# Optimization experiments

Hardware: AMD Instinct MI355X
Metric: run time of the kernel (lower is better)

Reference implementation:

```python
import jax, jax.numpy as jnp
import numpy as np

N_CID = 10000
N_TIME = 10000
SEQ_LEN = 4096
STATE_LEN = 4096


def setup_inputs() -> dict:
    key = jax.random.key(0)
    k1, k2, k3 = jax.random.split(key, 3)
    history = jax.random.randint(k1, (SEQ_LEN,), 0, N_TIME, dtype=jnp.int64)
    current = jax.random.randint(k2, (STATE_LEN,), 0, N_CID, dtype=jnp.int64)
    cid_time = jax.random.normal(k3, (N_CID, N_TIME), dtype=jnp.float32)
    return {"history": history, "current": current, "cid_time": cid_time}


def reference(history, current, cid_time):
    # Vectorized form of the double loop:
    # attn_energies[i, j] = cid_time[current[i], history[j]]
    attn_energies = cid_time[current][:, history]  # [state_len, seq_len]
    # F.softmax with no dim on a 2-D tensor -> softmax over last dim
    return jax.nn.softmax(attn_energies, axis=-1)
```

## Files before the change

kernel.cpp:

```cpp
#include <hip/hip_runtime.h>


constexpr int SEQ_LEN   = 4096;
constexpr int STATE_LEN = 4096;
constexpr int N_TIME    = 10000;
constexpr int THREADS   = 256;
constexpr int VPT       = SEQ_LEN / THREADS;
constexpr int V4PT      = VPT / 4;
constexpr int ROW_F4    = N_TIME / 4;

__global__ __launch_bounds__(THREADS) void attn_cid_time_kernel(
    const int*   __restrict__ history,
    const int*   __restrict__ current,
    const float* __restrict__ cid_time,
    float*       __restrict__ out)
{
    __shared__ float row[N_TIME];
    __shared__ float red[4];

    const int t   = threadIdx.x;
    const int rid = blockIdx.x;

    int4 hidx[V4PT];
    const int4* __restrict__ h4 = reinterpret_cast<const int4*>(history);
#pragma unroll
    for (int k = 0; k < V4PT; ++k)
        hidx[k] = h4[t + k * THREADS];

    const long long cid = (long long)current[rid];
    const float4* __restrict__ s4 =
        reinterpret_cast<const float4*>(cid_time + cid * (long long)N_TIME);
    float4* __restrict__ row4 = reinterpret_cast<float4*>(row);
    for (int i = t; i < ROW_F4; i += THREADS)
        row4[i] = s4[i];
    __syncthreads();

    float v[VPT];
    float m = -3.402823466e+38f;
#pragma unroll
    for (int k = 0; k < V4PT; ++k) {
        v[4*k + 0] = row[hidx[k].x];
        v[4*k + 1] = row[hidx[k].y];
        v[4*k + 2] = row[hidx[k].z];
        v[4*k + 3] = row[hidx[k].w];
        m = fmaxf(m, fmaxf(fmaxf(v[4*k+0], v[4*k+1]), fmaxf(v[4*k+2], v[4*k+3])));
    }

#pragma unroll
    for (int off = 32; off >= 1; off >>= 1)
        m = fmaxf(m, __shfl_xor(m, off, 64));
    const int wid  = t >> 6;
    const int lane = t & 63;
    if (lane == 0) red[wid] = m;
    __syncthreads();
    m = fmaxf(fmaxf(red[0], red[1]), fmaxf(red[2], red[3]));
    __syncthreads();

    float s = 0.0f;
#pragma unroll
    for (int k = 0; k < VPT; ++k) {
        const float e = __expf(v[k] - m);
        v[k] = e;
        s += e;
    }

#pragma unroll
    for (int off = 32; off >= 1; off >>= 1)
        s += __shfl_xor(s, off, 64);
    if (lane == 0) red[wid] = s;
    __syncthreads();
    s = (red[0] + red[1]) + (red[2] + red[3]);
    const float inv = 1.0f / s;

    float4* __restrict__ dst4 =
        reinterpret_cast<float4*>(out + (long long)rid * SEQ_LEN);
#pragma unroll
    for (int k = 0; k < V4PT; ++k) {
        float4 o;
        o.x = v[4*k + 0] * inv;
        o.y = v[4*k + 1] * inv;
        o.z = v[4*k + 2] * inv;
        o.w = v[4*k + 3] * inv;
        dst4[t + k * THREADS] = o;
    }
}

extern "C" void kernel_launch(void* const* d_in, const int* in_sizes, int n_in,
                              void* d_out, int out_size, void* d_ws, size_t ws_size,
                              hipStream_t stream) {
    const int*   history  = (const int*)d_in[0];
    const int*   current  = (const int*)d_in[1];
    const float* cid_time = (const float*)d_in[2];
    float*       out      = (float*)d_out;

    attn_cid_time_kernel<<<STATE_LEN, THREADS, 0, stream>>>(history, current, cid_time, out);
}
```

Before: 488.0 us.

## Stage gathered rows via global_load_lds and double block size to 512 threads

Each cid_time row is now copied straight from global memory into LDS with the 16-byte global_load_lds builtin, one 1 KB chunk per wave, plus a scalar tail loop for the leftover elements. This removes the round trip through VGPRs and the separate LDS store. The block grows from 256 to 512 threads with a launch-bounds occupancy hint, so more waves are in flight per row, and the reductions now loop over all eight waves. The cost is that each thread holds fewer values, and correctness relies on the compiler waiting for the async LDS loads before the barrier.

```diff
diff --git a/kernel.cpp b/kernel.cpp
--- a/kernel.cpp
+++ b/kernel.cpp
@@ -1,25 +1,32 @@
 #include <hip/hip_runtime.h>
 
 
-constexpr int SEQ_LEN   = 4096;
-constexpr int STATE_LEN = 4096;
-constexpr int N_TIME    = 10000;
-constexpr int THREADS   = 256;
-constexpr int VPT       = SEQ_LEN / THREADS;
-constexpr int V4PT      = VPT / 4;
-constexpr int ROW_F4    = N_TIME / 4;
+constexpr int SEQ_LEN    = 4096;
+constexpr int STATE_LEN  = 4096;
+constexpr int N_TIME     = 10000;
+constexpr int THREADS    = 512;
+constexpr int NWAVES     = THREADS / 64;
+constexpr int VPT        = SEQ_LEN / THREADS;
+constexpr int V4PT       = VPT / 4;
+constexpr int ROW_BYTES  = N_TIME * 4;
+constexpr int CHUNK      = 64 * 16;
+constexpr int NFULL      = ROW_BYTES / CHUNK;
+constexpr int TAIL_BASE  = (NFULL * CHUNK) / 4;
+constexpr int TAIL_ELEMS = N_TIME - TAIL_BASE;
 
-__global__ __launch_bounds__(THREADS) void attn_cid_time_kernel(
+__global__ __launch_bounds__(THREADS, 8) void attn_cid_time_kernel(
     const int*   __restrict__ history,
     const int*   __restrict__ current,
     const float* __restrict__ cid_time,
     float*       __restrict__ out)
 {
-    __shared__ float row[N_TIME];
-    __shared__ float red[4];
+    __shared__ alignas(16) float row[N_TIME];
+    __shared__ float red[NWAVES];
 
-    const int t   = threadIdx.x;
-    const int rid = blockIdx.x;
+    const int t    = threadIdx.x;
+    const int rid  = blockIdx.x;
+    const int wid  = t >> 6;
+    const int lane = t & 63;
 
     int4 hidx[V4PT];
     const int4* __restrict__ h4 = reinterpret_cast<const int4*>(history);
@@ -28,11 +35,18 @@
         hidx[k] = h4[t + k * THREADS];
 
     const long long cid = (long long)current[rid];
-    const float4* __restrict__ s4 =
-        reinterpret_cast<const float4*>(cid_time + cid * (long long)N_TIME);
-    float4* __restrict__ row4 = reinterpret_cast<float4*>(row);
-    for (int i = t; i < ROW_F4; i += THREADS)
-        row4[i] = s4[i];
+    const float* __restrict__ src = cid_time + cid * (long long)N_TIME;
+    const char*  srcb = reinterpret_cast<const char*>(src);
+    char*        rowb = reinterpret_cast<char*>(row);
+
+    for (int c = wid; c < NFULL; c += NWAVES) {
+        __builtin_amdgcn_global_load_lds(
+            (const __attribute__((address_space(1))) unsigned int*)(srcb + c * CHUNK + lane * 16),
+            (__attribute__((address_space(3))) unsigned int*)(rowb + c * CHUNK),
+            16, 0, 0);
+    }
+    if (t < TAIL_ELEMS)
+        row[TAIL_BASE + t] = src[TAIL_BASE + t];
     __syncthreads();
 
     float v[VPT];
@@ -49,11 +63,11 @@
 #pragma unroll
     for (int off = 32; off >= 1; off >>= 1)
         m = fmaxf(m, __shfl_xor(m, off, 64));
-    const int wid  = t >> 6;
-    const int lane = t & 63;
     if (lane == 0) red[wid] = m;
     __syncthreads();
-    m = fmaxf(fmaxf(red[0], red[1]), fmaxf(red[2], red[3]));
+#pragma unroll
+    for (int w = 0; w < NWAVES; ++w)
+        m = fmaxf(m, red[w]);
     __syncthreads();
 
     float s = 0.0f;
@@ -69,8 +83,11 @@
         s += __shfl_xor(s, off, 64);
     if (lane == 0) red[wid] = s;
     __syncthreads();
-    s = (red[0] + red[1]) + (red[2] + red[3]);
-    const float inv = 1.0f / s;
+    float tot = 0.0f;
+#pragma unroll
+    for (int w = 0; w < NWAVES; ++w)
+        tot += red[w];
+    const float inv = 1.0f / tot;
 
     float4* __restrict__ dst4 =
         reinterpret_cast<float4*>(out + (long long)rid * SEQ_LEN);
```

Result: no change. 486.2 us (-0.4%).
